# Kernel tuning notes

Hardware: AMD Instinct MI355X
Metric: run time of the kernel (lower is better)

## Reference

```python
import jax, jax.numpy as jnp
import numpy as np

D_MODEL = 256
N_HEADS = 8
HEAD_DIM = D_MODEL // N_HEADS  # 32
B, S = 8, 2048


def setup_inputs() -> dict:
    key = jax.random.key(0)
    ks = jax.random.split(key, 8)
    scale = 1.0 / np.sqrt(D_MODEL)
    return {
        "q": jax.random.normal(ks[0], (B, S, D_MODEL), jnp.float32),
        "k": jax.random.normal(ks[1], (B, S, D_MODEL), jnp.float32),
        "v": jax.random.normal(ks[2], (B, S, D_MODEL), jnp.float32),
        # padding mask: 1.0 = masked (added as -1e9), 0.0 = keep; shape (1,1,1,S)
        "m": jax.random.randint(ks[3], (1, 1, 1, S), 0, 2).astype(jnp.float32),
        "wq": jax.random.normal(ks[4], (D_MODEL, D_MODEL), jnp.float32) * scale,
        "bq": jnp.zeros((D_MODEL,), jnp.float32),
        "wk": jax.random.normal(ks[5], (D_MODEL, D_MODEL), jnp.float32) * scale,
        "bk": jnp.zeros((D_MODEL,), jnp.float32),
        "wv": jax.random.normal(ks[6], (D_MODEL, D_MODEL), jnp.float32) * scale,
        "bv": jnp.zeros((D_MODEL,), jnp.float32),
        "wo": jax.random.normal(ks[7], (D_MODEL, D_MODEL), jnp.float32) * scale,
        "bo": jnp.zeros((D_MODEL,), jnp.float32),
    }


def _split_heads(x):
    # (B, S, D) -> (B, H, S, dh)
    b, s, _ = x.shape
    return x.reshape(b, s, N_HEADS, HEAD_DIM).transpose(0, 2, 1, 3)


def reference(q, k, v, m, wq, bq, wk, bk, wv, bv, wo, bo):
    qh = _split_heads(q @ wq + bq)
    kh = _split_heads(k @ wk + bk)
    vh = _split_heads(v @ wv + bv)
    # scaled dot-product attention with additive padding mask
    logits = jnp.einsum("bhqd,bhkd->bhqk", qh, kh) / jnp.sqrt(
        jnp.asarray(HEAD_DIM, jnp.float32)
    )
    logits = logits + m * (-1e9)
    attn = jax.nn.softmax(logits, axis=-1)
    out = jnp.einsum("bhqk,bhkd->bhqd", attn, vh)  # (B, H, S, dh)
    out = out.transpose(0, 2, 1, 3).reshape(q.shape[0], -1, D_MODEL)
    return out @ wo + bo
```

## Files before the change

### kernel.cpp

```cpp
#include <hip/hip_runtime.h>

typedef short short8 __attribute__((ext_vector_type(8)));
typedef float f32x4 __attribute__((ext_vector_type(4)));
typedef float f32x16 __attribute__((ext_vector_type(16)));
typedef unsigned int uint2v __attribute__((ext_vector_type(2)));

#define NHEADS 8
#define DHEAD 32
#define DMODEL 256
#define SEQ 2048
#define QSCALE 0.17677669529663687f
#define LOG2E 1.4426950408889634f
#define NEGBIG -1.4427e9f
#define DEFER_THR 11.0f

__device__ __forceinline__ unsigned short f2bf(float x) {
  union { float f; unsigned int u; } c; c.f = x;
  return (unsigned short)((c.u + 0x7fffu + ((c.u >> 16) & 1u)) >> 16);
}

__device__ __forceinline__ unsigned int cvtpk(float lo, float hi) {
  unsigned int r;
  asm("v_cvt_pk_bf16_f32 %0, %1, %2" : "=v"(r) : "v"(lo), "v"(hi));
  return r;
}

__device__ __forceinline__ short8 pk8(float4 a, float4 b) {
  union { unsigned int u[4]; short8 s; } r;
  r.u[0] = cvtpk(a.x, a.y);
  r.u[1] = cvtpk(a.z, a.w);
  r.u[2] = cvtpk(b.x, b.y);
  r.u[3] = cvtpk(b.z, b.w);
  return r.s;
}

__device__ __forceinline__ float fexp2(float x) {
#if __has_builtin(__builtin_amdgcn_exp2f)
  return __builtin_amdgcn_exp2f(x);
#else
  return exp2f(x);
#endif
}

__device__ __forceinline__ uint2v plswap(unsigned int a, unsigned int b) {
#if __has_builtin(__builtin_amdgcn_permlane32_swap)
  return __builtin_amdgcn_permlane32_swap(a, b, false, false);
#else
  uint2v r;
  unsigned int sa = __shfl_xor(a, 32), sb = __shfl_xor(b, 32);
  int hi = (threadIdx.x & 63) >> 5;
  r[0] = hi ? sb : a;
  r[1] = hi ? b : sa;
  return r;
#endif
}

__device__ __forceinline__ int swz(int row, int c) {
  return row * 512 + ((c ^ (row & 7)) << 4);
}

__global__ __launch_bounds__(256) void prep_kernel(
    const float* __restrict__ wq, const float* __restrict__ wk,
    const float* __restrict__ wv, const float* __restrict__ wo,
    const float* __restrict__ bq, unsigned short* __restrict__ wt,
    float* __restrict__ bqs)
{
  __shared__ float tile[256][17];
  const int blk = blockIdx.x;
  const int mi = blk >> 4, nt = blk & 15;
  const float* w = (mi == 0) ? wq : (mi == 1) ? wk : (mi == 2) ? wv : wo;
  const float scale = (mi == 0) ? QSCALE * LOG2E : 1.0f;
  const int t = threadIdx.x;
  {
    const float* src = w + (size_t)t * DMODEL + nt * 16;
    #pragma unroll
    for (int i = 0; i < 16; i += 4) {
      float4 f = *(const float4*)(src + i);
      tile[t][i + 0] = f.x; tile[t][i + 1] = f.y;
      tile[t][i + 2] = f.z; tile[t][i + 3] = f.w;
    }
  }
  __syncthreads();
  unsigned short* dst = wt + mi * 65536 + nt * 4096;
  #pragma unroll
  for (int gi = 0; gi < 2; gi++) {
    const int g = t * 2 + gi;
    const int kk = g >> 6, l = g & 63;
    const int fr = l & 15, hi4 = l >> 4;
    union { unsigned short us[8]; uint4 u; } o;
    #pragma unroll
    for (int j = 0; j < 8; j++)
      o.us[j] = f2bf(tile[kk * 32 + hi4 * 8 + j][fr] * scale);
    *(uint4*)(dst + g * 8) = o.u;
  }
  if (blk == 0) bqs[t] = bq[t] * QSCALE * LOG2E;
}

__global__ __launch_bounds__(256) void scan_kernel(
    const float* __restrict__ m, int* __restrict__ cidx,
    float* __restrict__ tailbias, int* __restrict__ nkp)
{
  __shared__ int ssum[256];
  const int t = threadIdx.x;
  float mv[8];
  float4 m0 = *(const float4*)(m + t * 8);
  float4 m1 = *(const float4*)(m + t * 8 + 4);
  mv[0]=m0.x; mv[1]=m0.y; mv[2]=m0.z; mv[3]=m0.w;
  mv[4]=m1.x; mv[5]=m1.y; mv[6]=m1.z; mv[7]=m1.w;
  int keep[8], cnt = 0;
  #pragma unroll
  for (int j = 0; j < 8; j++) { keep[j] = (mv[j] == 0.0f); cnt += keep[j]; }
  ssum[t] = cnt;
  __syncthreads();
  for (int off = 1; off < 256; off <<= 1) {
    int add = (t >= off) ? ssum[t - off] : 0;
    __syncthreads();
    ssum[t] += add;
    __syncthreads();
  }
  int base = ssum[t] - cnt;
  const int nk = ssum[255];
  #pragma unroll
  for (int j = 0; j < 8; j++) {
    cidx[t * 8 + j] = keep[j] ? base : -1;
    base += keep[j];
  }
  if (t == 0) nkp[0] = nk;
  if (t < 32) {
    int g = (nk & ~31) + t;
    tailbias[t] = (g < nk) ? 0.0f : NEGBIG;
  }
}

__global__ __launch_bounds__(256) void qkv_kernel(
    const float* __restrict__ q, const float* __restrict__ k,
    const float* __restrict__ v, const unsigned short* __restrict__ wt,
    const float* __restrict__ bqs, const float* __restrict__ bk,
    const float* __restrict__ bv, const int* __restrict__ cidx,
    unsigned short* __restrict__ qf, unsigned short* __restrict__ kf,
    unsigned short* __restrict__ vf)
{
  __shared__ __align__(16) char alds[32768];
  const int z = blockIdx.y;
  const int tile = blockIdx.x;
  const int t = threadIdx.x;
  const int w = t >> 6, lane = t & 63;
  const int fr = lane & 15, hi4 = lane >> 4;

  const float* x = (z == 0) ? q : (z == 1) ? k : v;
  const float* xbase = x + (size_t)tile * 64 * DMODEL;

  #pragma unroll
  for (int i = 0; i < 8; i++) {
    const int gi = i * 256 + t;
    const int row = gi >> 5, c = gi & 31;
    const float4* src = (const float4*)(xbase + row * DMODEL + c * 8);
    float4 a0 = src[0], a1 = src[1];
    *(short8*)(alds + swz(row, c)) = pk8(a0, a1);
  }
  __syncthreads();

  f32x4 acc[4][4];
  #pragma unroll
  for (int mi = 0; mi < 4; mi++)
    #pragma unroll
    for (int ni = 0; ni < 4; ni++) { acc[mi][ni][0]=0.f; acc[mi][ni][1]=0.f; acc[mi][ni][2]=0.f; acc[mi][ni][3]=0.f; }

  const unsigned short* wz = wt + z * 65536 + (w * 4) * 4096;
  for (int kk = 0; kk < DMODEL; kk += 32) {
    short8 a[4], b[4];
    #pragma unroll
    for (int mi = 0; mi < 4; mi++)
      a[mi] = *(const short8*)(alds + swz(mi * 16 + fr, (kk >> 3) + hi4));
    #pragma unroll
    for (int ni = 0; ni < 4; ni++)
      b[ni] = *(const short8*)(wz + ni * 4096 + (kk >> 5) * 512 + lane * 8);
    #pragma unroll
    for (int mi = 0; mi < 4; mi++)
      #pragma unroll
      for (int ni = 0; ni < 4; ni++)
        acc[mi][ni] = __builtin_amdgcn_mfma_f32_16x16x32_bf16(a[mi], b[ni], acc[mi][ni], 0, 0, 0);
  }

  const float* bias = (z == 0) ? bqs : (z == 1) ? bk : bv;
  #pragma unroll
  for (int ni = 0; ni < 4; ni++) {
    const int f = w * 64 + ni * 16 + fr;
    const float bb = bias[f];
    const int h = f >> 5, d = f & 31;
    #pragma unroll
    for (int mi = 0; mi < 4; mi++) {
      #pragma unroll
      for (int j = 0; j < 4; j++) {
        const int token = tile * 64 + mi * 16 + hi4 * 4 + j;
        const int b_ = token >> 11, s = token & 2047;
        const unsigned short val = f2bf(acc[mi][ni][j] + bb);
        const size_t bhb = (size_t)(b_ * NHEADS + h) * 65536;
        if (z == 0) {
          qf[bhb + (s >> 5) * 1024 + (d >> 4) * 512 + ((d >> 3) & 1) * 256 + (s & 31) * 8 + (d & 7)] = val;
        } else {
          const int cs = cidx[s];
          if (cs >= 0) {
            if (z == 1)
              kf[bhb + (cs >> 5) * 1024 + (d >> 4) * 512 + ((d >> 3) & 1) * 256 + (cs & 31) * 8 + (d & 7)] = val;
            else
              vf[bhb + (cs >> 5) * 1024 + ((cs >> 4) & 1) * 512 + ((cs >> 3) & 1) * 256 + d * 8 + (cs & 7)] = val;
          }
        }
      }
    }
  }
}

template<bool MASKED>
__device__ __forceinline__ void attn_tile(
    const unsigned short* __restrict__ Kl, const unsigned short* __restrict__ Vl,
    int tb, const short8 qf0, const short8 qf1, const float* __restrict__ tailbias,
    int hi, f32x16& oacc, float& mrun, float& lrun)
{
  const short8 kf0 = *(const short8*)(Kl + tb);
  const short8 kf1 = *(const short8*)(Kl + tb + 512);
  f32x16 sacc;
  #pragma unroll
  for (int i = 0; i < 16; i++) sacc[i] = 0.0f;
  __builtin_amdgcn_s_setprio(1);
  sacc = __builtin_amdgcn_mfma_f32_32x32x16_bf16(kf0, qf0, sacc, 0, 0, 0);
  sacc = __builtin_amdgcn_mfma_f32_32x32x16_bf16(kf1, qf1, sacc, 0, 0, 0);
  __builtin_amdgcn_s_setprio(0);

  float p[16];
  if (MASKED) {
    const float4 t0 = *(const float4*)(tailbias + 4 * hi);
    const float4 t1 = *(const float4*)(tailbias + 4 * hi + 8);
    const float4 t2 = *(const float4*)(tailbias + 4 * hi + 16);
    const float4 t3 = *(const float4*)(tailbias + 4 * hi + 24);
    p[0]=sacc[0]+t0.x;  p[1]=sacc[1]+t0.y;  p[2]=sacc[2]+t0.z;  p[3]=sacc[3]+t0.w;
    p[4]=sacc[4]+t1.x;  p[5]=sacc[5]+t1.y;  p[6]=sacc[6]+t1.z;  p[7]=sacc[7]+t1.w;
    p[8]=sacc[8]+t2.x;  p[9]=sacc[9]+t2.y;  p[10]=sacc[10]+t2.z; p[11]=sacc[11]+t2.w;
    p[12]=sacc[12]+t3.x; p[13]=sacc[13]+t3.y; p[14]=sacc[14]+t3.z; p[15]=sacc[15]+t3.w;
  } else {
    #pragma unroll
    for (int i = 0; i < 16; i++) p[i] = sacc[i];
  }

  float x0 = fmaxf(fmaxf(p[0], p[1]), p[2]);
  float x1 = fmaxf(fmaxf(p[3], p[4]), p[5]);
  float x2 = fmaxf(fmaxf(p[6], p[7]), p[8]);
  float x3 = fmaxf(fmaxf(p[9], p[10]), p[11]);
  float x4 = fmaxf(fmaxf(p[12], p[13]), p[14]);
  float tmax = fmaxf(fmaxf(fmaxf(x0, x1), fmaxf(x2, x3)), fmaxf(x4, p[15]));

  if (!__all(tmax <= mrun + DEFER_THR)) {
    float pm = fmaxf(tmax, __shfl_xor(tmax, 32));
    float mnew = fmaxf(mrun, pm);
    float corr = fexp2(mrun - mnew);
    mrun = mnew;
    lrun *= corr;
    #pragma unroll
    for (int i = 0; i < 16; i++) oacc[i] *= corr;
  }

  float psum = 0.0f;
  #pragma unroll
  for (int i = 0; i < 16; i++) { p[i] = fexp2(p[i] - mrun); psum += p[i]; }
  lrun += psum;

  const unsigned int A0 = cvtpk(p[0], p[1]);
  const unsigned int A1 = cvtpk(p[2], p[3]);
  const unsigned int B0 = cvtpk(p[4], p[5]);
  const unsigned int B1 = cvtpk(p[6], p[7]);
  const unsigned int A2 = cvtpk(p[8], p[9]);
  const unsigned int A3 = cvtpk(p[10], p[11]);
  const unsigned int B2 = cvtpk(p[12], p[13]);
  const unsigned int B3 = cvtpk(p[14], p[15]);
  union { unsigned int u[4]; short8 s; } pb0, pb1;
  uint2v r0 = plswap(A0, B0); pb0.u[0] = r0[0]; pb0.u[2] = r0[1];
  uint2v r1 = plswap(A1, B1); pb0.u[1] = r1[0]; pb0.u[3] = r1[1];
  uint2v r2 = plswap(A2, B2); pb1.u[0] = r2[0]; pb1.u[2] = r2[1];
  uint2v r3 = plswap(A3, B3); pb1.u[1] = r3[0]; pb1.u[3] = r3[1];

  const short8 vf0 = *(const short8*)(Vl + tb);
  const short8 vf1 = *(const short8*)(Vl + tb + 512);
  __builtin_amdgcn_s_setprio(1);
  oacc = __builtin_amdgcn_mfma_f32_32x32x16_bf16(vf0, pb0.s, oacc, 0, 0, 0);
  oacc = __builtin_amdgcn_mfma_f32_32x32x16_bf16(vf1, pb1.s, oacc, 0, 0, 0);
  __builtin_amdgcn_s_setprio(0);
}

__global__ __launch_bounds__(256) void attn_kernel(
    const unsigned short* __restrict__ qf, const unsigned short* __restrict__ kfr,
    const unsigned short* __restrict__ vfr, const float* __restrict__ tailbias,
    const int* __restrict__ nkp, unsigned short* __restrict__ attno)
{
  const int bid = blockIdx.x;
  const int L = (bid & 7) * 128 + (bid >> 3);
  const int bh = L >> 4, qt = L & 15;
  const int w = threadIdx.x >> 6, lane = threadIdx.x & 63;
  const int ql = lane & 31, hi = lane >> 5;
  const int qrow = qt * 128 + w * 32 + ql;
  const int loff = hi * 256 + ql * 8;
  const unsigned short* Qb = qf + (size_t)bh * 65536 + (size_t)(qt * 4 + w) * 1024 + loff;
  const unsigned short* Kl = kfr + (size_t)bh * 65536 + loff;
  const unsigned short* Vl = vfr + (size_t)bh * 65536 + loff;

  const short8 q0 = *(const short8*)(Qb);
  const short8 q1 = *(const short8*)(Qb + 512);

  f32x16 oacc;
  #pragma unroll
  for (int i = 0; i < 16; i++) oacc[i] = 0.0f;
  float mrun = -1e30f, lrun = 0.0f;

  const int nk = *nkp;
  const int nfull = nk >> 5, ntail = nk & 31;

  for (int ti = 0; ti < nfull; ti++)
    attn_tile<false>(Kl, Vl, ti * 1024, q0, q1, tailbias, hi, oacc, mrun, lrun);
  if (ntail)
    attn_tile<true>(Kl, Vl, nfull * 1024, q0, q1, tailbias, hi, oacc, mrun, lrun);

  const float ltot = lrun + __shfl_xor(lrun, 32);
  const float inv = 1.0f / ltot;
  const int b = bh >> 3, h = bh & 7;
  unsigned short* orow = attno + ((size_t)(b * SEQ + qrow)) * DMODEL + h * DHEAD + 4 * hi;
  #pragma unroll
  for (int g = 0; g < 4; g++) {
    union { unsigned short us[4]; uint2 u2; } st;
    st.us[0] = f2bf(oacc[4 * g + 0] * inv);
    st.us[1] = f2bf(oacc[4 * g + 1] * inv);
    st.us[2] = f2bf(oacc[4 * g + 2] * inv);
    st.us[3] = f2bf(oacc[4 * g + 3] * inv);
    *(uint2*)(orow + 8 * g) = st.u2;
  }
}

__global__ __launch_bounds__(256) void oproj_kernel(
    const unsigned short* __restrict__ attno, const unsigned short* __restrict__ wto,
    const float* __restrict__ bo, float* __restrict__ out)
{
  __shared__ __align__(16) char alds[16384];
  const int tile = blockIdx.x;
  const int t = threadIdx.x;
  const int w = t >> 6, lane = t & 63;
  const int fr = lane & 15, hi4 = lane >> 4;
  const unsigned short* abase = attno + (size_t)tile * 32 * DMODEL;

  #pragma unroll
  for (int i = 0; i < 4; i++) {
    const int gi = i * 256 + t;
    const int row = gi >> 5, c = gi & 31;
    uint4 u = *(const uint4*)(abase + row * DMODEL + c * 8);
    *(uint4*)(alds + swz(row, c)) = u;
  }
  __syncthreads();

  f32x4 acc[2][4];
  #pragma unroll
  for (int mi = 0; mi < 2; mi++)
    #pragma unroll
    for (int ni = 0; ni < 4; ni++) { acc[mi][ni][0]=0.f; acc[mi][ni][1]=0.f; acc[mi][ni][2]=0.f; acc[mi][ni][3]=0.f; }

  const unsigned short* wz = wto + (w * 4) * 4096;
  for (int kk = 0; kk < DMODEL; kk += 32) {
    short8 a[2], b[4];
    #pragma unroll
    for (int mi = 0; mi < 2; mi++)
      a[mi] = *(const short8*)(alds + swz(mi * 16 + fr, (kk >> 3) + hi4));
    #pragma unroll
    for (int ni = 0; ni < 4; ni++)
      b[ni] = *(const short8*)(wz + ni * 4096 + (kk >> 5) * 512 + lane * 8);
    #pragma unroll
    for (int mi = 0; mi < 2; mi++)
      #pragma unroll
      for (int ni = 0; ni < 4; ni++)
        acc[mi][ni] = __builtin_amdgcn_mfma_f32_16x16x32_bf16(a[mi], b[ni], acc[mi][ni], 0, 0, 0);
  }

  #pragma unroll
  for (int ni = 0; ni < 4; ni++) {
    const int f = w * 64 + ni * 16 + fr;
    const float bb = bo[f];
    #pragma unroll
    for (int mi = 0; mi < 2; mi++) {
      #pragma unroll
      for (int j = 0; j < 4; j++) {
        const int token = tile * 32 + mi * 16 + hi4 * 4 + j;
        out[(size_t)token * DMODEL + f] = acc[mi][ni][j] + bb;
      }
    }
  }
}

extern "C" void kernel_launch(void* const* d_in, const int* in_sizes, int n_in,
                              void* d_out, int out_size, void* d_ws, size_t ws_size,
                              hipStream_t stream) {
  const float* q  = (const float*)d_in[0];
  const float* k  = (const float*)d_in[1];
  const float* v  = (const float*)d_in[2];
  const float* m  = (const float*)d_in[3];
  const float* wq = (const float*)d_in[4];
  const float* bq = (const float*)d_in[5];
  const float* wk = (const float*)d_in[6];
  const float* bk = (const float*)d_in[7];
  const float* wv = (const float*)d_in[8];
  const float* bv = (const float*)d_in[9];
  const float* wo = (const float*)d_in[10];
  const float* bo = (const float*)d_in[11];
  float* out = (float*)d_out;

  char* ws = (char*)d_ws;
  unsigned short* wt    = (unsigned short*)ws;
  float* bqs            = (float*)(ws + 524288);
  float* tailbias       = (float*)(ws + 525312);
  int*   nkp            = (int*)(ws + 525440);
  int*   cidx           = (int*)(ws + 526336);
  unsigned short* qf    = (unsigned short*)(ws + 1048576);
  unsigned short* kfr   = qf + 4194304;
  unsigned short* vfr   = kfr + 4194304;
  unsigned short* attno = vfr + 4194304;

  prep_kernel<<<dim3(64), dim3(256), 0, stream>>>(wq, wk, wv, wo, bq, wt, bqs);
  scan_kernel<<<dim3(1), dim3(256), 0, stream>>>(m, cidx, tailbias, nkp);
  qkv_kernel<<<dim3(256, 3), dim3(256), 0, stream>>>(q, k, v, wt, bqs, bk, bv, cidx, qf, kfr, vfr);
  attn_kernel<<<dim3(1024), dim3(256), 0, stream>>>(qf, kfr, vfr, tailbias, nkp, attno);
  oproj_kernel<<<dim3(512), dim3(256), 0, stream>>>(attno, wt + 3 * 65536, bo, out);
}
```

Baseline: 180.1 us.

## Prefetch K/V tiles, fold max into MFMA init, compute row sums via MFMA

The attention loop now loads the next K/V tile into registers while the current tile computes, hiding global load latency. The running max is folded into the score accumulator's initial value (-mrun), so no per-element subtraction is needed. The row sum is computed by an extra MFMA against a ones vector instead of VALU adds and a cross-lane shuffle. Q/K projection stores are transposed so each lane writes packed 4-element bf16 chunks instead of scalar stores. The cost is more MFMA work per tile and higher register pressure from the prefetch buffers.

```diff
diff --git a/kernel.cpp b/kernel.cpp
--- a/kernel.cpp
+++ b/kernel.cpp
@@ -175,36 +175,65 @@
     #pragma unroll
     for (int ni = 0; ni < 4; ni++)
       b[ni] = *(const short8*)(wz + ni * 4096 + (kk >> 5) * 512 + lane * 8);
-    #pragma unroll
-    for (int mi = 0; mi < 4; mi++)
+    if (z < 2) {
       #pragma unroll
-      for (int ni = 0; ni < 4; ni++)
-        acc[mi][ni] = __builtin_amdgcn_mfma_f32_16x16x32_bf16(a[mi], b[ni], acc[mi][ni], 0, 0, 0);
-  }
-
-  const float* bias = (z == 0) ? bqs : (z == 1) ? bk : bv;
-  #pragma unroll
-  for (int ni = 0; ni < 4; ni++) {
-    const int f = w * 64 + ni * 16 + fr;
-    const float bb = bias[f];
-    const int h = f >> 5, d = f & 31;
+      for (int mi = 0; mi < 4; mi++)
+        #pragma unroll
+        for (int ni = 0; ni < 4; ni++)
+          acc[mi][ni] = __builtin_amdgcn_mfma_f32_16x16x32_bf16(b[ni], a[mi], acc[mi][ni], 0, 0, 0);
+    } else {
+      #pragma unroll
+      for (int mi = 0; mi < 4; mi++)
+        #pragma unroll
+        for (int ni = 0; ni < 4; ni++)
+          acc[mi][ni] = __builtin_amdgcn_mfma_f32_16x16x32_bf16(a[mi], b[ni], acc[mi][ni], 0, 0, 0);
+    }
+  }
+
+  if (z < 2) {
+    const float* bias = (z == 0) ? bqs : bk;
+    unsigned short* dstbuf = (z == 0) ? qf : kf;
+    float4 bias4[4];
+    #pragma unroll
+    for (int ni = 0; ni < 4; ni++)
+      bias4[ni] = *(const float4*)(bias + w * 64 + ni * 16 + hi4 * 4);
     #pragma unroll
     for (int mi = 0; mi < 4; mi++) {
+      const int tok = tile * 64 + mi * 16 + fr;
+      const int b_ = tok >> 11, sl = tok & 2047;
+      const int cs = (z == 0) ? sl : cidx[sl];
+      if (cs >= 0) {
+        #pragma unroll
+        for (int ni = 0; ni < 4; ni++) {
+          const int f0 = w * 64 + ni * 16 + hi4 * 4;
+          const int h = f0 >> 5, dq = f0 & 31;
+          uint2 val;
+          val.x = cvtpk(acc[mi][ni][0] + bias4[ni].x, acc[mi][ni][1] + bias4[ni].y);
+          val.y = cvtpk(acc[mi][ni][2] + bias4[ni].z, acc[mi][ni][3] + bias4[ni].w);
+          const size_t off = (size_t)(b_ * NHEADS + h) * 65536
+                           + (cs >> 5) * 1024 + ((dq >> 4) & 1) * 512 + ((dq >> 3) & 1) * 256
+                           + (cs & 31) * 8 + (dq & 7);
+          *(uint2*)(dstbuf + off) = val;
+        }
+      }
+    }
+  } else {
+    #pragma unroll
+    for (int ni = 0; ni < 4; ni++) {
+      const int f = w * 64 + ni * 16 + fr;
+      const float bb = bv[f];
+      const int h = f >> 5, d = f & 31;
       #pragma unroll
-      for (int j = 0; j < 4; j++) {
-        const int token = tile * 64 + mi * 16 + hi4 * 4 + j;
-        const int b_ = token >> 11, s = token & 2047;
-        const unsigned short val = f2bf(acc[mi][ni][j] + bb);
-        const size_t bhb = (size_t)(b_ * NHEADS + h) * 65536;
-        if (z == 0) {
-          qf[bhb + (s >> 5) * 1024 + (d >> 4) * 512 + ((d >> 3) & 1) * 256 + (s & 31) * 8 + (d & 7)] = val;
-        } else {
+      for (int mi = 0; mi < 4; mi++) {
+        #pragma unroll
+        for (int j = 0; j < 4; j++) {
+          const int token = tile * 64 + mi * 16 + hi4 * 4 + j;
+          const int b_ = token >> 11, s = token & 2047;
           const int cs = cidx[s];
           if (cs >= 0) {
-            if (z == 1)
-              kf[bhb + (cs >> 5) * 1024 + (d >> 4) * 512 + ((d >> 3) & 1) * 256 + (cs & 31) * 8 + (d & 7)] = val;
-            else
-              vf[bhb + (cs >> 5) * 1024 + ((cs >> 4) & 1) * 512 + ((cs >> 3) & 1) * 256 + d * 8 + (cs & 7)] = val;
+            vf[(size_t)(b_ * NHEADS + h) * 65536
+               + (cs >> 5) * 1024 + ((cs >> 4) & 1) * 512 + ((cs >> 3) & 1) * 256
+               + d * 8 + (cs & 7)] = f2bf(acc[mi][ni][j] + bb);
           }
         }
       }
@@ -214,18 +243,16 @@
 
 template<bool MASKED>
 __device__ __forceinline__ void attn_tile(
-    const unsigned short* __restrict__ Kl, const unsigned short* __restrict__ Vl,
-    int tb, const short8 qf0, const short8 qf1, const float* __restrict__ tailbias,
-    int hi, f32x16& oacc, float& mrun, float& lrun)
-{
-  const short8 kf0 = *(const short8*)(Kl + tb);
-  const short8 kf1 = *(const short8*)(Kl + tb + 512);
+    short8 kf0, short8 kf1, short8 vf0, short8 vf1, short8 onesf,
+    short8 q0, short8 q1, const float* __restrict__ tailbias,
+    int hi, f32x16& oacc, f32x16& lacc, float& mrun)
+{
   f32x16 sacc;
   #pragma unroll
-  for (int i = 0; i < 16; i++) sacc[i] = 0.0f;
+  for (int i = 0; i < 16; i++) sacc[i] = -mrun;
   __builtin_amdgcn_s_setprio(1);
-  sacc = __builtin_amdgcn_mfma_f32_32x32x16_bf16(kf0, qf0, sacc, 0, 0, 0);
-  sacc = __builtin_amdgcn_mfma_f32_32x32x16_bf16(kf1, qf1, sacc, 0, 0, 0);
+  sacc = __builtin_amdgcn_mfma_f32_32x32x16_bf16(kf0, q0, sacc, 0, 0, 0);
+  sacc = __builtin_amdgcn_mfma_f32_32x32x16_bf16(kf1, q1, sacc, 0, 0, 0);
   __builtin_amdgcn_s_setprio(0);
 
   float p[16];
@@ -250,20 +277,20 @@
   float x4 = fmaxf(fmaxf(p[12], p[13]), p[14]);
   float tmax = fmaxf(fmaxf(fmaxf(x0, x1), fmaxf(x2, x3)), fmaxf(x4, p[15]));
 
-  if (!__all(tmax <= mrun + DEFER_THR)) {
+  if (!__all(tmax <= DEFER_THR)) {
     float pm = fmaxf(tmax, __shfl_xor(tmax, 32));
-    float mnew = fmaxf(mrun, pm);
-    float corr = fexp2(mrun - mnew);
-    mrun = mnew;
-    lrun *= corr;
+    float delta = fmaxf(pm, 0.0f);
+    float corr = fexp2(-delta);
+    mrun += delta;
+    lacc[0] *= corr;
     #pragma unroll
     for (int i = 0; i < 16; i++) oacc[i] *= corr;
-  }
-
-  float psum = 0.0f;
-  #pragma unroll
-  for (int i = 0; i < 16; i++) { p[i] = fexp2(p[i] - mrun); psum += p[i]; }
-  lrun += psum;
+    #pragma unroll
+    for (int i = 0; i < 16; i++) p[i] -= delta;
+  }
+
+  #pragma unroll
+  for (int i = 0; i < 16; i++) p[i] = fexp2(p[i]);
 
   const unsigned int A0 = cvtpk(p[0], p[1]);
   const unsigned int A1 = cvtpk(p[2], p[3]);
@@ -279,9 +306,9 @@
   uint2v r2 = plswap(A2, B2); pb1.u[0] = r2[0]; pb1.u[2] = r2[1];
   uint2v r3 = plswap(A3, B3); pb1.u[1] = r3[0]; pb1.u[3] = r3[1];
 
-  const short8 vf0 = *(const short8*)(Vl + tb);
-  const short8 vf1 = *(const short8*)(Vl + tb + 512);
   __builtin_amdgcn_s_setprio(1);
+  lacc = __builtin_amdgcn_mfma_f32_32x32x16_bf16(onesf, pb0.s, lacc, 0, 0, 0);
+  lacc = __builtin_amdgcn_mfma_f32_32x32x16_bf16(onesf, pb1.s, lacc, 0, 0, 0);
   oacc = __builtin_amdgcn_mfma_f32_32x32x16_bf16(vf0, pb0.s, oacc, 0, 0, 0);
   oacc = __builtin_amdgcn_mfma_f32_32x32x16_bf16(vf1, pb1.s, oacc, 0, 0, 0);
   __builtin_amdgcn_s_setprio(0);
@@ -306,21 +333,39 @@
   const short8 q0 = *(const short8*)(Qb);
   const short8 q1 = *(const short8*)(Qb + 512);
 
-  f32x16 oacc;
-  #pragma unroll
-  for (int i = 0; i < 16; i++) oacc[i] = 0.0f;
-  float mrun = -1e30f, lrun = 0.0f;
+  short8 onesf;
+  #pragma unroll
+  for (int i = 0; i < 8; i++) onesf[i] = (short)0x3F80;
+
+  f32x16 oacc, lacc;
+  #pragma unroll
+  for (int i = 0; i < 16; i++) { oacc[i] = 0.0f; lacc[i] = 0.0f; }
+  float mrun = 0.0f;
 
   const int nk = *nkp;
   const int nfull = nk >> 5, ntail = nk & 31;
-
-  for (int ti = 0; ti < nfull; ti++)
-    attn_tile<false>(Kl, Vl, ti * 1024, q0, q1, tailbias, hi, oacc, mrun, lrun);
+  const int ntiles = nfull + (ntail ? 1 : 0);
+
+  short8 ck0, ck1, cv0, cv1;
+  if (ntiles > 0) {
+    ck0 = *(const short8*)(Kl);
+    ck1 = *(const short8*)(Kl + 512);
+    cv0 = *(const short8*)(Vl);
+    cv1 = *(const short8*)(Vl + 512);
+  }
+  for (int ti = 0; ti < nfull; ti++) {
+    const int nb = (ti + 1 < ntiles ? ti + 1 : ti) * 1024;
+    short8 nk0 = *(const short8*)(Kl + nb);
+    short8 nk1 = *(const short8*)(Kl + nb + 512);
+    short8 nv0 = *(const short8*)(Vl + nb);
+    short8 nv1 = *(const short8*)(Vl + nb + 512);
+    attn_tile<false>(ck0, ck1, cv0, cv1, onesf, q0, q1, tailbias, hi, oacc, lacc, mrun);
+    ck0 = nk0; ck1 = nk1; cv0 = nv0; cv1 = nv1;
+  }
   if (ntail)
-    attn_tile<true>(Kl, Vl, nfull * 1024, q0, q1, tailbias, hi, oacc, mrun, lrun);
-
-  const float ltot = lrun + __shfl_xor(lrun, 32);
-  const float inv = 1.0f / ltot;
+    attn_tile<true>(ck0, ck1, cv0, cv1, onesf, q0, q1, tailbias, hi, oacc, lacc, mrun);
+
+  const float inv = 1.0f / lacc[0];
   const int b = bh >> 3, h = bh & 7;
   unsigned short* orow = attno + ((size_t)(b * SEQ + qrow)) * DMODEL + h * DHEAD + 4 * hi;
   #pragma unroll
```

New measurement: 181.8 us. About the same (+0.9%).
